# Performance work log

Hardware: AMD Instinct MI355X
Metric: run time of the kernel (lower is better)

## Reference

```python
import jax, jax.numpy as jnp
import numpy as np
import math

CHANNELS = 1024
NUM_HEADS = 16
HEAD_DIM = CHANNELS // NUM_HEADS  # 64
ROPE_DIM = int(HEAD_DIM * 0.5)    # 32
BASE_FREQ = 10000.0


def apply_rope(x):
    """x: [b, h, t, d]; rotate first ROPE_DIM features, pass the rest through."""
    t = x.shape[2]
    half = ROPE_DIM // 2
    theta = 1.0 / (BASE_FREQ ** (jnp.arange(0, ROPE_DIM, 2, dtype=jnp.float32) / ROPE_DIM))  # [half]
    ang = jnp.arange(t, dtype=jnp.float32)[:, None] * theta[None, :]  # [t, half]
    ang = jnp.concatenate([ang, ang], axis=-1)  # [t, ROPE_DIM]
    cos = jnp.cos(ang)[None, None, :, :]
    sin = jnp.sin(ang)[None, None, :, :]
    x_rope, x_pass = x[..., :ROPE_DIM], x[..., ROPE_DIM:]
    neg_half = jnp.concatenate([-x_rope[..., half:], x_rope[..., :half]], axis=-1)
    x_rope = x_rope * cos + neg_half * sin
    return jnp.concatenate([x_rope, x_pass], axis=-1)


def proximal_bias(length):
    pos = jnp.arange(length, dtype=jnp.float32)
    diff = pos[None, :] - pos[:, None]
    return -jnp.log1p(jnp.abs(diff))[None, None, :, :]  # [1,1,t,t]


def conv1x1(x, w, b):
    """x: [b, c_in, t], w: [c_out, c_in], b: [c_out] -> [b, c_out, t]"""
    return jnp.einsum('oc,bct->bot', w, x) + b[None, :, None]


def setup_inputs() -> dict:
    key = jax.random.key(0)
    ks = jax.random.split(key, 10)
    B, C, T = 8, CHANNELS, 1024
    scale = 1.0 / math.sqrt(C)
    return {
        "x": jax.random.normal(ks[0], (B, C, T), dtype=jnp.float32),
        "context": jax.random.normal(ks[1], (B, C, T), dtype=jnp.float32),
        "attention_mask": jnp.ones((B, 1, 1, T), dtype=jnp.int32),
        "Wq": jax.random.normal(ks[2], (C, C), dtype=jnp.float32) * scale,
        "bq": jnp.zeros((C,), dtype=jnp.float32),
        "Wk": jax.random.normal(ks[3], (C, C), dtype=jnp.float32) * scale,
        "bk": jnp.zeros((C,), dtype=jnp.float32),
        "Wv": jax.random.normal(ks[4], (C, C), dtype=jnp.float32) * scale,
        "bv": jnp.zeros((C,), dtype=jnp.float32),
        "Wo": jax.random.normal(ks[5], (C, C), dtype=jnp.float32) * scale,
        "bo": jnp.zeros((C,), dtype=jnp.float32),
    }


def reference(x, context, attention_mask, Wq, bq, Wk, bk, Wv, bv, Wo, bo):
    B, C, T = x.shape
    H, D = NUM_HEADS, HEAD_DIM
    q = conv1x1(x, Wq, bq)
    k = conv1x1(context, Wk, bk)
    v = conv1x1(context, Wv, bv)
    # b (h d) t -> b h t d
    def split_heads(z):
        return z.reshape(B, H, D, -1).transpose(0, 1, 3, 2)
    q, k, v = split_heads(q), split_heads(k), split_heads(v)
    q = apply_rope(q)
    k = apply_rope(k)
    scores = jnp.einsum('bhqd,bhkd->bhqk', q, k) / math.sqrt(D)
    scores = scores + proximal_bias(T)  # proximal_bias=True, self-attention
    scores = jnp.where(attention_mask == 0, jnp.float32(-10000.0), scores)
    probs = jax.nn.softmax(scores, axis=-1)  # dropout_rate=0.0 -> identity
    out = jnp.einsum('bhqk,bhkd->bhqd', probs, v)
    # b h q d -> b (h d) q
    out = out.transpose(0, 1, 3, 2).reshape(B, C, T)
    return conv1x1(out, Wo, bo)
```

## Files before the change

### kernel.cpp

```cpp
#include <hip/hip_runtime.h>
#include <hip/hip_bf16.h>
#include <math.h>

#define BB 8
#define CC 1024
#define TT 1024
#define HH 16
#define DD 64

typedef __attribute__((ext_vector_type(8))) short short8;
typedef __attribute__((ext_vector_type(4))) short short4_;
typedef __attribute__((ext_vector_type(4))) float f32x4;

#define QSCALE 0.18033688f

__device__ __forceinline__ unsigned short f2bf(float f) {
    unsigned u = __builtin_bit_cast(unsigned, f);
    u += 0x7fffu + ((u >> 16) & 1u);
    return (unsigned short)(u >> 16);
}

__device__ __forceinline__ f32x4 mfma16(short8 a, short8 b, f32x4 c) {
    return __builtin_amdgcn_mfma_f32_16x16x32_bf16(a, b, c, 0, 0, 0);
}

__device__ __forceinline__ void async16(const void* g, void* l) {
    __builtin_amdgcn_global_load_lds(
        (const __attribute__((address_space(1))) unsigned int*)g,
        (__attribute__((address_space(3))) unsigned int*)l, 16, 0, 0);
}

template<int CTRL>
__device__ __forceinline__ float dpp_mv(float x) {
    return __builtin_bit_cast(float,
        __builtin_amdgcn_update_dpp(0, __builtin_bit_cast(int, x),
                                    CTRL, 0xF, 0xF, false));
}
__device__ __forceinline__ float rowsum16(float x) {
    x += dpp_mv<0xB1>(x);
    x += dpp_mv<0x4E>(x);
    x += dpp_mv<0x141>(x);
    x += dpp_mv<0x140>(x);
    return x;
}

__global__ __launch_bounds__(256) void cast_w_kernel(
    const float* __restrict__ Wq, const float* __restrict__ Wk,
    const float* __restrict__ Wv, const float* __restrict__ Wo,
    unsigned short* __restrict__ dst)
{
    const int z = blockIdx.y;
    const float* W = (z == 0) ? Wq : (z == 1) ? Wk : (z == 2) ? Wv : Wo;
    unsigned short* d = dst + (size_t)z * CC * CC;
    int idx = blockIdx.x * 256 + threadIdx.x;
    float4 f = ((const float4*)W)[idx];
    short4_ s;
    s[0] = (short)f2bf(f.x); s[1] = (short)f2bf(f.y);
    s[2] = (short)f2bf(f.z); s[3] = (short)f2bf(f.w);
    ((short4_*)d)[idx] = s;
}

__global__ __launch_bounds__(256) void tcast_kernel(
    const float* __restrict__ in, unsigned short* __restrict__ out)
{
    __shared__ float sT[64][65];
    const int tid = threadIdx.x;
    const int tB = blockIdx.x * 64, cT = blockIdx.y * 64, b = blockIdx.z;

    const float* ib = in + ((size_t)b * CC + cT) * TT + tB;
    const int r = tid >> 2;
    #pragma unroll
    for (int j = 0; j < 4; j++) {
        int t4 = (tid & 3) * 4 + j * 16;
        float4 f = *(const float4*)(ib + (size_t)r * TT + t4);
        sT[r][t4 + 0] = f.x; sT[r][t4 + 1] = f.y;
        sT[r][t4 + 2] = f.z; sT[r][t4 + 3] = f.w;
    }
    __syncthreads();
    const int t_l = tid >> 2, cch = (tid & 3) * 16;
    short8 o0, o1;
    #pragma unroll
    for (int i = 0; i < 8; i++) {
        o0[i] = (short)f2bf(sT[cch + i][t_l]);
        o1[i] = (short)f2bf(sT[cch + 8 + i][t_l]);
    }
    unsigned short* dp = out + ((size_t)b * TT + tB + t_l) * CC + cT + cch;
    *(short8*)dp = o0;
    *(short8*)(dp + 8) = o1;
}

__global__ __launch_bounds__(256) void qkv_gll_kernel(
    const unsigned short* __restrict__ inT,
    const unsigned short* __restrict__ Wq2, const unsigned short* __restrict__ Wk2,
    const unsigned short* __restrict__ Wv2,
    const float* __restrict__ bq, const float* __restrict__ bk,
    const float* __restrict__ bv,
    unsigned short* __restrict__ qo, unsigned short* __restrict__ ko,
    unsigned short* __restrict__ vo,
    int wbase, int nw)
{
    __shared__ __align__(16) short smem[4 * 64 * 72];
    short* sA = smem;
    short* sB = smem + 4096;

    const int tid = threadIdx.x, lane = tid & 63, wave = tid >> 6;
    const int wm = wave >> 1, wn = wave & 1;
    const int l15 = lane & 15, lq = lane >> 4;

    const int tTile = blockIdx.x, oTile = blockIdx.y;
    const int zz = blockIdx.z;
    const int w = wbase + ((nw == 2) ? (zz & 1) : 0);
    const int b = (nw == 2) ? (zz >> 1) : zz;
    const int oBase = oTile * 128, tBase = tTile * 128;

    const unsigned short* WA = (w == 0) ? Wq2 : (w == 1) ? Wk2 : Wv2;
    const float* bias        = (w == 0) ? bq  : (w == 1) ? bk  : bv;

    const int srow = lane >> 2;
    const int sch  = (lane ^ (lane >> 2) ^ (lane >> 4)) & 3;
    const unsigned short* gA0 = WA + (size_t)(oBase + wave * 32 + srow) * CC + sch * 8;
    const unsigned short* gA1 = gA0 + (size_t)16 * CC;
    const unsigned short* gB0 = inT + ((size_t)b * TT + tBase + wave * 32 + srow) * CC + sch * 8;
    const unsigned short* gB1 = gB0 + (size_t)16 * CC;
    short* lA0 = sA + (wave * 2 + 0) * 512;
    short* lA1 = sA + (wave * 2 + 1) * 512;
    short* lB0 = sB + (wave * 2 + 0) * 512;
    short* lB1 = sB + (wave * 2 + 1) * 512;

    const int csw = ((lq ^ (l15 & 3) ^ (l15 >> 2)) & 3) * 8;

    f32x4 acc[4][4];
    #pragma unroll
    for (int mt = 0; mt < 4; mt++)
        #pragma unroll
        for (int nt = 0; nt < 4; nt++) acc[mt][nt] = (f32x4){0.f, 0.f, 0.f, 0.f};

    for (int c0 = 0; c0 < CC; c0 += 32) {
        async16(gA0 + c0, lA0);
        async16(gA1 + c0, lA1);
        async16(gB0 + c0, lB0);
        async16(gB1 + c0, lB1);
        __syncthreads();

        short8 af[4], bf[4];
        #pragma unroll
        for (int mt = 0; mt < 4; mt++)
            af[mt] = *(short8*)(sA + (wm * 64 + mt * 16 + l15) * 32 + csw);
        #pragma unroll
        for (int nt = 0; nt < 4; nt++)
            bf[nt] = *(short8*)(sB + (wn * 64 + nt * 16 + l15) * 32 + csw);
        #pragma unroll
        for (int mt = 0; mt < 4; mt++)
            #pragma unroll
            for (int nt = 0; nt < 4; nt++)
                acc[mt][nt] = mfma16(af[mt], bf[nt], acc[mt][nt]);
        __syncthreads();
    }

    #pragma unroll
    for (int mt = 0; mt < 4; mt++)
        #pragma unroll
        for (int r = 0; r < 4; r++) {
            float bi = bias[oBase + wm * 64 + mt * 16 + lq * 4 + r];
            #pragma unroll
            for (int nt = 0; nt < 4; nt++) {
                acc[mt][nt][r] += bi;
                if (w == 0) acc[mt][nt][r] *= QSCALE;
            }
        }

    const int h = oTile * 2 + wm;
    short* sT = smem + wave * (64 * 72);

    if (w < 2) {
        #pragma unroll
        for (int r = 0; r < 4; r++) {
            float theta = powf(10000.0f, -(float)(lq * 4 + r) * (1.0f / 16.0f));
            #pragma unroll
            for (int nt = 0; nt < 4; nt++) {
                float tpos = (float)(tBase + wn * 64 + nt * 16 + l15);
                float sa, ca;
                sincosf(tpos * theta, &sa, &ca);
                float x0 = acc[0][nt][r], x1 = acc[1][nt][r];
                acc[0][nt][r] = x0 * ca - x1 * sa;
                acc[1][nt][r] = x1 * ca + x0 * sa;
            }
        }
        #pragma unroll
        for (int nt = 0; nt < 4; nt++)
            #pragma unroll
            for (int mt = 0; mt < 4; mt++) {
                short4_ v4;
                #pragma unroll
                for (int r = 0; r < 4; r++) v4[r] = (short)f2bf(acc[mt][nt][r]);
                *(short4_*)(sT + (nt * 16 + l15) * 72 + mt * 16 + lq * 4) = v4;
            }
    } else {
        #pragma unroll
        for (int mt = 0; mt < 4; mt++)
            #pragma unroll
            for (int r = 0; r < 4; r++)
                #pragma unroll
                for (int nt = 0; nt < 4; nt++)
                    sT[(mt * 16 + lq * 4 + r) * 72 + nt * 16 + l15] =
                        (short)f2bf(acc[mt][nt][r]);
    }
    __asm__ volatile("s_waitcnt lgkmcnt(0)" ::: "memory");

    unsigned short* dstBase;
    if (w == 0)
        dstBase = qo + ((size_t)(b * HH + h) * TT + tBase + wn * 64 + lane) * DD;
    else if (w == 1)
        dstBase = ko + ((size_t)(b * HH + h) * TT + tBase + wn * 64 + lane) * DD;
    else
        dstBase = vo + ((size_t)(b * HH + h) * DD + lane) * TT + tBase + wn * 64;
    #pragma unroll
    for (int j = 0; j < 8; j++)
        *(short8*)(dstBase + j * 8) = *(short8*)(sT + lane * 72 + j * 8);
}

__global__ __launch_bounds__(256) void oproj_gll_kernel(
    const unsigned short* __restrict__ att, const unsigned short* __restrict__ Wo2,
    const float* __restrict__ bo, float* __restrict__ out)
{
    __shared__ __align__(16) short smem[8192];
    short* sA = smem;
    short* sB = smem + 4096;

    const int tid = threadIdx.x, lane = tid & 63, wave = tid >> 6;
    const int wm = wave >> 1, wn = wave & 1;
    const int l15 = lane & 15, lq = lane >> 4;
    const int tTile = blockIdx.x, oTile = blockIdx.y, b = blockIdx.z;
    const int oBase = oTile * 128, tBase = tTile * 128;

    const int srow = lane >> 2;
    const int sch  = (lane ^ (lane >> 2) ^ (lane >> 4)) & 3;
    const unsigned short* gA0 = Wo2 + (size_t)(oBase + wave * 32 + srow) * CC + sch * 8;
    const unsigned short* gA1 = gA0 + (size_t)16 * CC;
    const unsigned short* attB = att + (size_t)b * HH * TT * DD;
    const int t0 = tBase + wave * 32 + srow;
    short* lA0 = sA + (wave * 2 + 0) * 512;
    short* lA1 = sA + (wave * 2 + 1) * 512;
    short* lB0 = sB + (wave * 2 + 0) * 512;
    short* lB1 = sB + (wave * 2 + 1) * 512;

    const int csw = ((lq ^ (l15 & 3) ^ (l15 >> 2)) & 3) * 8;

    f32x4 acc[4][4];
    #pragma unroll
    for (int mt = 0; mt < 4; mt++)
        #pragma unroll
        for (int nt = 0; nt < 4; nt++) acc[mt][nt] = (f32x4){0.f, 0.f, 0.f, 0.f};

    for (int c0 = 0; c0 < CC; c0 += 32) {
        int c = c0 + sch * 8;
        const unsigned short* g0 =
            attB + ((size_t)(c >> 6) * TT + t0) * DD + (c & 63);
        async16(gA0 + c0, lA0);
        async16(gA1 + c0, lA1);
        async16(g0, lB0);
        async16(g0 + 16 * DD, lB1);
        __syncthreads();

        short8 af[4], bf[4];
        #pragma unroll
        for (int mt = 0; mt < 4; mt++)
            af[mt] = *(short8*)(sA + (wm * 64 + mt * 16 + l15) * 32 + csw);
        #pragma unroll
        for (int nt = 0; nt < 4; nt++)
            bf[nt] = *(short8*)(sB + (wn * 64 + nt * 16 + l15) * 32 + csw);
        #pragma unroll
        for (int mt = 0; mt < 4; mt++)
            #pragma unroll
            for (int nt = 0; nt < 4; nt++)
                acc[mt][nt] = mfma16(af[mt], bf[nt], acc[mt][nt]);
        __syncthreads();
    }

    #pragma unroll
    for (int mt = 0; mt < 4; mt++)
        #pragma unroll
        for (int r = 0; r < 4; r++) {
            int o = oBase + wm * 64 + mt * 16 + lq * 4 + r;
            float bi = bo[o];
            float* dst = out + ((size_t)b * CC + o) * TT + tBase + wn * 64;
            #pragma unroll
            for (int nt = 0; nt < 4; nt++)
                dst[nt * 16 + l15] = acc[mt][nt][r] + bi;
        }
}

__global__ __launch_bounds__(256) void attn_mfma_kernel(
    const unsigned short* __restrict__ q, const unsigned short* __restrict__ k,
    const unsigned short* __restrict__ v, const int* __restrict__ mask,
    unsigned short* __restrict__ att)
{
    __shared__ __align__(16) short sQ[64 * 72];
    __shared__ __align__(16) short sK[64 * 72];
    __shared__ __align__(16) short sV[64 * 72];
    __shared__ __align__(16) short sP[64 * 72];

    const int tid = threadIdx.x, lane = tid & 63, wq = tid >> 6;
    const int l15 = lane & 15, lq = lane >> 4;
    const int qTile = blockIdx.x, bh = blockIdx.y, b = bh >> 4;

    const int sr = tid >> 2, sc = (tid & 3) * 16;

    {
        const unsigned short* gq = q + ((size_t)bh * TT + qTile * 64 + sr) * DD + sc;
        *(short8*)(sQ + sr * 72 + sc)     = *(const short8*)gq;
        *(short8*)(sQ + sr * 72 + sc + 8) = *(const short8*)(gq + 8);
    }
    __syncthreads();

    const short8 aq0 = *(short8*)(sQ + (wq * 16 + l15) * 72 + lq * 8);
    const short8 aq1 = *(short8*)(sQ + (wq * 16 + l15) * 72 + 32 + lq * 8);

    f32x4 accO[4];
    float l_i[4];
    #pragma unroll
    for (int r = 0; r < 4; r++) {
        l_i[r] = 0.f;
        accO[r] = (f32x4){0.f, 0.f, 0.f, 0.f};
    }

    const int qpos0 = qTile * 64 + wq * 16 + lq * 4;
    const int* maskB = mask + b * TT;
    const unsigned short* kB = k + (size_t)bh * TT * DD;
    const unsigned short* vB = v + (size_t)bh * DD * TT;

    for (int kt = 0; kt < 16; kt++) {
        const unsigned short* gk = kB + (size_t)(kt * 64 + sr) * DD + sc;
        short8 k0 = *(const short8*)gk;
        short8 k1 = *(const short8*)(gk + 8);
        const unsigned short* gv = vB + (size_t)sr * TT + kt * 64 + sc;
        short8 v0 = *(const short8*)gv;
        short8 v1 = *(const short8*)(gv + 8);

        __syncthreads();
        *(short8*)(sK + sr * 72 + sc)     = k0;
        *(short8*)(sK + sr * 72 + sc + 8) = k1;
        *(short8*)(sV + sr * 72 + sc)     = v0;
        *(short8*)(sV + sr * 72 + sc + 8) = v1;
        __syncthreads();

        f32x4 s4[4];
        #pragma unroll
        for (int nt = 0; nt < 4; nt++) {
            short8 b0 = *(short8*)(sK + (nt * 16 + l15) * 72 + lq * 8);
            short8 b1 = *(short8*)(sK + (nt * 16 + l15) * 72 + 32 + lq * 8);
            f32x4 z = (f32x4){0.f, 0.f, 0.f, 0.f};
            z = mfma16(aq0, b0, z);
            z = mfma16(aq1, b1, z);
            s4[nt] = z;
        }

        float p[4][4];
        float rr[4] = {0.f, 0.f, 0.f, 0.f};
        #pragma unroll
        for (int nt = 0; nt < 4; nt++) {
            int kpos = kt * 64 + nt * 16 + l15;
            int mk = maskB[kpos];
            float fb = (float)(kpos - qpos0);
            #pragma unroll
            for (int r = 0; r < 4; r++) {
                float ad = 1.0f + fabsf(fb - (float)r);
                float rd = __builtin_amdgcn_rcpf(ad);
                float pe = exp2f(s4[nt][r]) * rd;
                pe = mk ? pe : 0.f;
                p[nt][r] = pe;
                rr[r] += pe;
            }
        }
        #pragma unroll
        for (int r = 0; r < 4; r++)
            l_i[r] += rowsum16(rr[r]);

        #pragma unroll
        for (int nt = 0; nt < 4; nt++)
            #pragma unroll
            for (int r = 0; r < 4; r++) {
                unsigned u = __builtin_bit_cast(unsigned, p[nt][r]);
                sP[(wq * 16 + lq * 4 + r) * 72 + nt * 16 + l15] =
                    (short)((u + 0x8000u) >> 16);
            }
        __asm__ volatile("s_waitcnt lgkmcnt(0)" ::: "memory");

        short8 ap0 = *(short8*)(sP + (wq * 16 + l15) * 72 + lq * 8);
        short8 ap1 = *(short8*)(sP + (wq * 16 + l15) * 72 + 32 + lq * 8);
        #pragma unroll
        for (int nt = 0; nt < 4; nt++) {
            short8 b0 = *(short8*)(sV + (nt * 16 + l15) * 72 + lq * 8);
            short8 b1 = *(short8*)(sV + (nt * 16 + l15) * 72 + 32 + lq * 8);
            accO[nt] = mfma16(ap0, b0, accO[nt]);
            accO[nt] = mfma16(ap1, b1, accO[nt]);
        }
    }

    unsigned short* aB = att + ((size_t)bh * TT + qTile * 64 + wq * 16 + lq * 4) * DD;
    #pragma unroll
    for (int r = 0; r < 4; r++) {
        float inv = 1.0f / l_i[r];
        #pragma unroll
        for (int nt = 0; nt < 4; nt++)
            aB[(size_t)r * DD + nt * 16 + l15] = f2bf(accO[nt][r] * inv);
    }
}

__global__ __launch_bounds__(256) void qkv_mfma_kernel(
    const float* __restrict__ x, const float* __restrict__ ctx,
    const float* __restrict__ Wq, const float* __restrict__ bq,
    const float* __restrict__ Wk, const float* __restrict__ bk,
    const float* __restrict__ Wv, const float* __restrict__ bv,
    unsigned short* __restrict__ qo, unsigned short* __restrict__ ko,
    unsigned short* __restrict__ vo)
{
    __shared__ __align__(16) short smem[4 * 64 * 72];
    short* sA = smem;
    short* sB = smem + 128 * 40;

    const int tid  = threadIdx.x;
    const int lane = tid & 63;
    const int wave = tid >> 6;
    const int wm = wave >> 1, wn = wave & 1;
    const int l15 = lane & 15, lq = lane >> 4;

    const int tTile = blockIdx.x, oTile = blockIdx.y;
    const int b = blockIdx.z / 3, w = blockIdx.z % 3;
    const int oBase = oTile * 128, tBase = tTile * 128;

    const float* In   = (w == 0) ? x  : ctx;
    const float* W    = (w == 0) ? Wq : (w == 1) ? Wk : Wv;
    const float* bias = (w == 0) ? bq : (w == 1) ? bk : bv;
    const float* InB  = In + (size_t)b * CC * TT;

    const int ao = tid >> 1, ak = (tid & 1) * 16;
    const int bt = tid & 127, bk_ = (tid >> 7) * 16;
    const float* gA = W + (size_t)(oBase + ao) * CC + ak;
    const float* gB = InB + (size_t)bk_ * TT + tBase + bt;

    f32x4 acc[4][4];
    #pragma unroll
    for (int mt = 0; mt < 4; mt++)
        #pragma unroll
        for (int nt = 0; nt < 4; nt++) acc[mt][nt] = (f32x4){0.f, 0.f, 0.f, 0.f};

    for (int c0 = 0; c0 < CC; c0 += 32) {
        float fa[16], fb[16];
        #pragma unroll
        for (int i = 0; i < 4; i++) {
            float4 t4 = *(const float4*)(gA + c0 + 4 * i);
            fa[4*i+0] = t4.x; fa[4*i+1] = t4.y; fa[4*i+2] = t4.z; fa[4*i+3] = t4.w;
        }
        #pragma unroll
        for (int j = 0; j < 16; j++)
            fb[j] = gB[(size_t)(c0 + j) * TT];

        __syncthreads();
        short8 pa0, pa1, pb0, pb1;
        #pragma unroll
        for (int e = 0; e < 8; e++) {
            pa0[e] = (short)f2bf(fa[e]);   pa1[e] = (short)f2bf(fa[8 + e]);
            pb0[e] = (short)f2bf(fb[e]);   pb1[e] = (short)f2bf(fb[8 + e]);
        }
        *(short8*)(sA + ao * 40 + ak)     = pa0;
        *(short8*)(sA + ao * 40 + ak + 8) = pa1;
        *(short8*)(sB + bt * 40 + bk_)     = pb0;
        *(short8*)(sB + bt * 40 + bk_ + 8) = pb1;
        __syncthreads();

        short8 af[4], bf[4];
        #pragma unroll
        for (int mt = 0; mt < 4; mt++)
            af[mt] = *(short8*)(sA + (wm * 64 + mt * 16 + l15) * 40 + lq * 8);
        #pragma unroll
        for (int nt = 0; nt < 4; nt++)
            bf[nt] = *(short8*)(sB + (wn * 64 + nt * 16 + l15) * 40 + lq * 8);
        #pragma unroll
        for (int mt = 0; mt < 4; mt++)
            #pragma unroll
            for (int nt = 0; nt < 4; nt++)
                acc[mt][nt] = mfma16(af[mt], bf[nt], acc[mt][nt]);
    }

    #pragma unroll
    for (int mt = 0; mt < 4; mt++)
        #pragma unroll
        for (int r = 0; r < 4; r++) {
            float bi = bias[oBase + wm * 64 + mt * 16 + lq * 4 + r];
            #pragma unroll
            for (int nt = 0; nt < 4; nt++) {
                acc[mt][nt][r] += bi;
                if (w == 0) acc[mt][nt][r] *= QSCALE;
            }
        }

    const int h = oTile * 2 + wm;
    __syncthreads();
    short* sT = smem + wave * (64 * 72);

    if (w < 2) {
        #pragma unroll
        for (int r = 0; r < 4; r++) {
            float theta = powf(10000.0f, -(float)(lq * 4 + r) * (1.0f / 16.0f));
            #pragma unroll
            for (int nt = 0; nt < 4; nt++) {
                float tpos = (float)(tBase + wn * 64 + nt * 16 + l15);
                float sa, ca;
                sincosf(tpos * theta, &sa, &ca);
                float x0 = acc[0][nt][r], x1 = acc[1][nt][r];
                acc[0][nt][r] = x0 * ca - x1 * sa;
                acc[1][nt][r] = x1 * ca + x0 * sa;
            }
        }
        #pragma unroll
        for (int nt = 0; nt < 4; nt++)
            #pragma unroll
            for (int mt = 0; mt < 4; mt++) {
                short4_ v4;
                #pragma unroll
                for (int r = 0; r < 4; r++) v4[r] = (short)f2bf(acc[mt][nt][r]);
                *(short4_*)(sT + (nt * 16 + l15) * 72 + mt * 16 + lq * 4) = v4;
            }
    } else {
        #pragma unroll
        for (int mt = 0; mt < 4; mt++)
            #pragma unroll
            for (int r = 0; r < 4; r++)
                #pragma unroll
                for (int nt = 0; nt < 4; nt++)
                    sT[(mt * 16 + lq * 4 + r) * 72 + nt * 16 + l15] =
                        (short)f2bf(acc[mt][nt][r]);
    }
    __asm__ volatile("s_waitcnt lgkmcnt(0)" ::: "memory");

    unsigned short* dstBase;
    if (w == 0)
        dstBase = qo + ((size_t)(b * HH + h) * TT + tBase + wn * 64 + lane) * DD;
    else if (w == 1)
        dstBase = ko + ((size_t)(b * HH + h) * TT + tBase + wn * 64 + lane) * DD;
    else
        dstBase = vo + ((size_t)(b * HH + h) * DD + lane) * TT + tBase + wn * 64;
    #pragma unroll
    for (int j = 0; j < 8; j++)
        *(short8*)(dstBase + j * 8) = *(short8*)(sT + lane * 72 + j * 8);
}

__global__ __launch_bounds__(256) void oproj_mfma_kernel(
    const unsigned short* __restrict__ att, const float* __restrict__ Wo,
    const float* __restrict__ bo, float* __restrict__ out)
{
    __shared__ __align__(16) short smem[2 * 128 * 40];
    short* sA = smem;
    short* sB = smem + 128 * 40;

    const int tid = threadIdx.x, lane = tid & 63, wave = tid >> 6;
    const int wm = wave >> 1, wn = wave & 1;
    const int l15 = lane & 15, lq = lane >> 4;
    const int tTile = blockIdx.x, oTile = blockIdx.y, b = blockIdx.z;
    const int oBase = oTile * 128, tBase = tTile * 128;

    const int ao = tid >> 1, ak = (tid & 1) * 16;
    const int bt = tid & 127, bk_ = (tid >> 7) * 16;
    const float* gA = Wo + (size_t)(oBase + ao) * CC + ak;

    f32x4 acc[4][4];
    #pragma unroll
    for (int mt = 0; mt < 4; mt++)
        #pragma unroll
        for (int nt = 0; nt < 4; nt++) acc[mt][nt] = (f32x4){0.f, 0.f, 0.f, 0.f};

    for (int c0 = 0; c0 < CC; c0 += 32) {
        float fa[16];
        #pragma unroll
        for (int i = 0; i < 4; i++) {
            float4 t4 = *(const float4*)(gA + c0 + 4 * i);
            fa[4*i+0] = t4.x; fa[4*i+1] = t4.y; fa[4*i+2] = t4.z; fa[4*i+3] = t4.w;
        }
        int c = c0 + bk_;
        const unsigned short* gB =
            att + (((size_t)b * HH + (c >> 6)) * TT + tBase + bt) * DD + (c & 63);
        short8 pb0 = *(const short8*)gB;
        short8 pb1 = *(const short8*)(gB + 8);

        __syncthreads();
        short8 pa0, pa1;
        #pragma unroll
        for (int e = 0; e < 8; e++) {
            pa0[e] = (short)f2bf(fa[e]); pa1[e] = (short)f2bf(fa[8 + e]);
        }
        *(short8*)(sA + ao * 40 + ak)      = pa0;
        *(short8*)(sA + ao * 40 + ak + 8)  = pa1;
        *(short8*)(sB + bt * 40 + bk_)     = pb0;
        *(short8*)(sB + bt * 40 + bk_ + 8) = pb1;
        __syncthreads();

        short8 af[4], bf[4];
        #pragma unroll
        for (int mt = 0; mt < 4; mt++)
            af[mt] = *(short8*)(sA + (wm * 64 + mt * 16 + l15) * 40 + lq * 8);
        #pragma unroll
        for (int nt = 0; nt < 4; nt++)
            bf[nt] = *(short8*)(sB + (wn * 64 + nt * 16 + l15) * 40 + lq * 8);
        #pragma unroll
        for (int mt = 0; mt < 4; mt++)
            #pragma unroll
            for (int nt = 0; nt < 4; nt++)
                acc[mt][nt] = mfma16(af[mt], bf[nt], acc[mt][nt]);
    }

    #pragma unroll
    for (int mt = 0; mt < 4; mt++)
        #pragma unroll
        for (int r = 0; r < 4; r++) {
            int o = oBase + wm * 64 + mt * 16 + lq * 4 + r;
            float bi = bo[o];
            float* dst = out + ((size_t)b * CC + o) * TT + tBase + wn * 64;
            #pragma unroll
            for (int nt = 0; nt < 4; nt++)
                dst[nt * 16 + l15] = acc[mt][nt][r] + bi;
        }
}

extern "C" void kernel_launch(void* const* d_in, const int* in_sizes, int n_in,
                              void* d_out, int out_size, void* d_ws, size_t ws_size,
                              hipStream_t stream)
{
    const float* x   = (const float*)d_in[0];
    const float* ctx = (const float*)d_in[1];
    const int* mask  = (const int*)d_in[2];
    const float* Wq  = (const float*)d_in[3];
    const float* bq  = (const float*)d_in[4];
    const float* Wk  = (const float*)d_in[5];
    const float* bk  = (const float*)d_in[6];
    const float* Wv  = (const float*)d_in[7];
    const float* bv  = (const float*)d_in[8];
    const float* Wo  = (const float*)d_in[9];
    const float* bo  = (const float*)d_in[10];
    float* out = (float*)d_out;

    const size_t nq = (size_t)BB * HH * TT * DD;
    const size_t nw = (size_t)CC * CC;

    if (ws_size >= (4 * nq + 4 * nw) * sizeof(unsigned short)) {
        unsigned short* q   = (unsigned short*)d_ws;
        unsigned short* k   = q + nq;
        unsigned short* v   = k + nq;
        unsigned short* buf = v + nq;
        unsigned short* Wb  = buf + nq;
        unsigned short* Wqb = Wb;
        unsigned short* Wkb = Wb + nw;
        unsigned short* Wvb = Wb + 2 * nw;
        unsigned short* Wob = Wb + 3 * nw;

        cast_w_kernel<<<dim3(1024, 4), 256, 0, stream>>>(Wq, Wk, Wv, Wo, Wb);
        tcast_kernel<<<dim3(16, 16, BB), 256, 0, stream>>>(x, buf);
        qkv_gll_kernel<<<dim3(8, 8, BB), 256, 0, stream>>>(
            buf, Wqb, Wkb, Wvb, bq, bk, bv, q, k, v, 0, 1);
        tcast_kernel<<<dim3(16, 16, BB), 256, 0, stream>>>(ctx, buf);
        qkv_gll_kernel<<<dim3(8, 8, BB * 2), 256, 0, stream>>>(
            buf, Wqb, Wkb, Wvb, bq, bk, bv, q, k, v, 1, 2);
        attn_mfma_kernel<<<dim3(TT / 64, BB * HH), 256, 0, stream>>>(
            q, k, v, mask, buf);
        oproj_gll_kernel<<<dim3(8, 8, BB), 256, 0, stream>>>(buf, Wob, bo, out);
    } else {
        unsigned short* q   = (unsigned short*)d_ws;
        unsigned short* k   = q + nq;
        unsigned short* v   = k + nq;
        unsigned short* att = v + nq;
        qkv_mfma_kernel<<<dim3(8, 8, BB * 3), 256, 0, stream>>>(
            x, ctx, Wq, bq, Wk, bk, Wv, bv, q, k, v);
        attn_mfma_kernel<<<dim3(TT / 64, BB * HH), 256, 0, stream>>>(
            q, k, v, mask, att);
        oproj_mfma_kernel<<<dim3(8, 8, BB), 256, 0, stream>>>(att, Wo, bo, out);
    }
}
```

Before: 357.7 us.

## Merge QKV projections into one launch and defer softmax row-sum reduction

When the workspace is large enough, x and context are transposed into separate buffers so that one qkv launch computes Q, K and V together. This cuts a launch and gives a larger grid. In the attention kernel, the per-tile row-sum shuffle reduction is deferred to the end, and P values are written straight to a sP buffer with a 68-short padded stride. The new path needs extra workspace; if the workspace is too small, the old path runs instead. The new padding could change LDS bank conflicts.

After: 351.5 us. No clear change (-1.7%).

```diff
diff --git a/kernel.cpp b/kernel.cpp
--- a/kernel.cpp
+++ b/kernel.cpp
@@ -90,14 +90,14 @@
 }
 
 __global__ __launch_bounds__(256) void qkv_gll_kernel(
-    const unsigned short* __restrict__ inT,
+    const unsigned short* __restrict__ xT, const unsigned short* __restrict__ cT,
     const unsigned short* __restrict__ Wq2, const unsigned short* __restrict__ Wk2,
     const unsigned short* __restrict__ Wv2,
     const float* __restrict__ bq, const float* __restrict__ bk,
     const float* __restrict__ bv,
     unsigned short* __restrict__ qo, unsigned short* __restrict__ ko,
     unsigned short* __restrict__ vo,
-    int wbase, int nw)
+    int mode)
 {
     __shared__ __align__(16) short smem[4 * 64 * 72];
     short* sA = smem;
@@ -109,8 +109,11 @@
 
     const int tTile = blockIdx.x, oTile = blockIdx.y;
     const int zz = blockIdx.z;
-    const int w = wbase + ((nw == 2) ? (zz & 1) : 0);
-    const int b = (nw == 2) ? (zz >> 1) : zz;
+    int w, b;
+    if (mode == 0)      { w = zz % 3;        b = zz / 3;  }
+    else if (mode == 1) { w = 0;             b = zz;      }
+    else                { w = 1 + (zz & 1);  b = zz >> 1; }
+    const unsigned short* inT = (w == 0) ? xT : cT;
     const int oBase = oTile * 128, tBase = tTile * 128;
 
     const unsigned short* WA = (w == 0) ? Wq2 : (w == 1) ? Wk2 : Wv2;
@@ -298,7 +301,7 @@
     __shared__ __align__(16) short sQ[64 * 72];
     __shared__ __align__(16) short sK[64 * 72];
     __shared__ __align__(16) short sV[64 * 72];
-    __shared__ __align__(16) short sP[64 * 72];
+    __shared__ __align__(16) short sP[64 * 68];
 
     const int tid = threadIdx.x, lane = tid & 63, wq = tid >> 6;
     const int l15 = lane & 15, lq = lane >> 4;
@@ -317,10 +320,10 @@
     const short8 aq1 = *(short8*)(sQ + (wq * 16 + l15) * 72 + 32 + lq * 8);
 
     f32x4 accO[4];
-    float l_i[4];
+    float l_acc[4];
     #pragma unroll
     for (int r = 0; r < 4; r++) {
-        l_i[r] = 0.f;
+        l_acc[r] = 0.f;
         accO[r] = (f32x4){0.f, 0.f, 0.f, 0.f};
     }
 
@@ -355,8 +358,6 @@
             s4[nt] = z;
         }
 
-        float p[4][4];
-        float rr[4] = {0.f, 0.f, 0.f, 0.f};
         #pragma unroll
         for (int nt = 0; nt < 4; nt++) {
             int kpos = kt * 64 + nt * 16 + l15;
@@ -368,26 +369,16 @@
                 float rd = __builtin_amdgcn_rcpf(ad);
                 float pe = exp2f(s4[nt][r]) * rd;
                 pe = mk ? pe : 0.f;
-                p[nt][r] = pe;
-                rr[r] += pe;
-            }
-        }
-        #pragma unroll
-        for (int r = 0; r < 4; r++)
-            l_i[r] += rowsum16(rr[r]);
-
-        #pragma unroll
-        for (int nt = 0; nt < 4; nt++)
-            #pragma unroll
-            for (int r = 0; r < 4; r++) {
-                unsigned u = __builtin_bit_cast(unsigned, p[nt][r]);
-                sP[(wq * 16 + lq * 4 + r) * 72 + nt * 16 + l15] =
+                l_acc[r] += pe;
+                unsigned u = __builtin_bit_cast(unsigned, pe);
+                sP[(wq * 16 + lq * 4 + r) * 68 + nt * 16 + l15] =
                     (short)((u + 0x8000u) >> 16);
             }
+        }
         __asm__ volatile("s_waitcnt lgkmcnt(0)" ::: "memory");
 
-        short8 ap0 = *(short8*)(sP + (wq * 16 + l15) * 72 + lq * 8);
-        short8 ap1 = *(short8*)(sP + (wq * 16 + l15) * 72 + 32 + lq * 8);
+        short8 ap0 = *(short8*)(sP + (wq * 16 + l15) * 68 + lq * 8);
+        short8 ap1 = *(short8*)(sP + (wq * 16 + l15) * 68 + 32 + lq * 8);
         #pragma unroll
         for (int nt = 0; nt < 4; nt++) {
             short8 b0 = *(short8*)(sV + (nt * 16 + l15) * 72 + lq * 8);
@@ -400,7 +391,7 @@
     unsigned short* aB = att + ((size_t)bh * TT + qTile * 64 + wq * 16 + lq * 4) * DD;
     #pragma unroll
     for (int r = 0; r < 4; r++) {
-        float inv = 1.0f / l_i[r];
+        float inv = 1.0f / rowsum16(l_acc[r]);
         #pragma unroll
         for (int nt = 0; nt < 4; nt++)
             aB[(size_t)r * DD + nt * 16 + l15] = f2bf(accO[nt][r] * inv);
@@ -642,7 +633,27 @@
     const size_t nq = (size_t)BB * HH * TT * DD;
     const size_t nw = (size_t)CC * CC;
 
-    if (ws_size >= (4 * nq + 4 * nw) * sizeof(unsigned short)) {
+    if (ws_size >= (5 * nq + 4 * nw) * sizeof(unsigned short)) {
+        unsigned short* q   = (unsigned short*)d_ws;
+        unsigned short* k   = q + nq;
+        unsigned short* v   = k + nq;
+        unsigned short* xT  = v + nq;
+        unsigned short* cT  = xT + nq;
+        unsigned short* Wb  = cT + nq;
+        unsigned short* Wqb = Wb;
+        unsigned short* Wkb = Wb + nw;
+        unsigned short* Wvb = Wb + 2 * nw;
+        unsigned short* Wob = Wb + 3 * nw;
+
+        cast_w_kernel<<<dim3(1024, 4), 256, 0, stream>>>(Wq, Wk, Wv, Wo, Wb);
+        tcast_kernel<<<dim3(16, 16, BB), 256, 0, stream>>>(x, xT);
+        tcast_kernel<<<dim3(16, 16, BB), 256, 0, stream>>>(ctx, cT);
+        qkv_gll_kernel<<<dim3(8, 8, BB * 3), 256, 0, stream>>>(
+            xT, cT, Wqb, Wkb, Wvb, bq, bk, bv, q, k, v, 0);
+        attn_mfma_kernel<<<dim3(TT / 64, BB * HH), 256, 0, stream>>>(
+            q, k, v, mask, xT);
+        oproj_gll_kernel<<<dim3(8, 8, BB), 256, 0, stream>>>(xT, Wob, bo, out);
+    } else if (ws_size >= (4 * nq + 4 * nw) * sizeof(unsigned short)) {
         unsigned short* q   = (unsigned short*)d_ws;
         unsigned short* k   = q + nq;
         unsigned short* v   = k + nq;
@@ -656,10 +667,10 @@
         cast_w_kernel<<<dim3(1024, 4), 256, 0, stream>>>(Wq, Wk, Wv, Wo, Wb);
         tcast_kernel<<<dim3(16, 16, BB), 256, 0, stream>>>(x, buf);
         qkv_gll_kernel<<<dim3(8, 8, BB), 256, 0, stream>>>(
-            buf, Wqb, Wkb, Wvb, bq, bk, bv, q, k, v, 0, 1);
+            buf, buf, Wqb, Wkb, Wvb, bq, bk, bv, q, k, v, 1);
         tcast_kernel<<<dim3(16, 16, BB), 256, 0, stream>>>(ctx, buf);
         qkv_gll_kernel<<<dim3(8, 8, BB * 2), 256, 0, stream>>>(
-            buf, Wqb, Wkb, Wvb, bq, bk, bv, q, k, v, 1, 2);
+            buf, buf, Wqb, Wkb, Wvb, bq, bk, bv, q, k, v, 2);
         attn_mfma_kernel<<<dim3(TT / 64, BB * HH), 256, 0, stream>>>(
             q, k, v, mask, buf);
         oproj_gll_kernel<<<dim3(8, 8, BB), 256, 0, stream>>>(buf, Wob, bo, out);
```
